# Optimization experiments

Measured on AMD Instinct MI355X. Metric: run time of the kernel, lower is better.

Reference implementation:

```python
import jax, jax.numpy as jnp
import numpy as np

B, T, N, D, H, M = 2, 12, 325, 64, 8, 3
EPS = 1e-6


def _layer_norm(x, g, b):
    mu = jnp.mean(x, axis=-1, keepdims=True)
    var = jnp.mean(jnp.square(x - mu), axis=-1, keepdims=True)
    return (x - mu) * jax.lax.rsqrt(var + EPS) * g + b


def _meta_w(ste, W1, b1, W2, b2):
    # ste: (b,t,n,d) -> per-token weight matrix (b,t,n,d,d)  [Meta_projection]
    h = jax.nn.relu(jnp.einsum('btnd,de->btne', ste, W1) + b1)
    w = jnp.einsum('btnd,df->btnf', h, W2) + b2
    b_, t_, n_, _ = ste.shape
    return w.reshape(b_, t_, n_, D, D)


def _meta_qkv(q, k, v, ste_q, ste_k, ste_v, mW1, mb1, mW2, mb2):
    wq = _meta_w(ste_q, mW1[0], mb1[0], mW2[0], mb2[0])
    wk = _meta_w(ste_k, mW1[1], mb1[1], mW2[1], mb2[1])
    wv = _meta_w(ste_v, mW1[2], mb1[2], mW2[2], mb2[2])
    mg = lambda x, w: jnp.einsum('btnd,btnde->btne', x, w)  # meta_guide
    return mg(q, wq), mg(k, wk), mg(v, wv)


def _split_heads(x):  # (B,L,d) -> (H*B,L,d/H), head-major = tf.concat(tf.split(x,H,-1),0)
    return jnp.concatenate(jnp.split(x, H, axis=-1), axis=0)


def _concat_heads(x):
    return jnp.concatenate(jnp.split(x, H, axis=0), axis=-1)


def _sdpa(q, k, v, tm=None):
    dk = q.shape[-1]
    scores = jnp.einsum('bqd,bkd->bqk', q, k) / jnp.sqrt(jnp.float32(dk))
    if tm is not None:  # spatial mask (n,n) broadcast over batch*heads
        scores = jnp.where(tm[None] > 0, scores, jnp.float32(-1e9))
    att = jax.nn.softmax(scores, axis=-1)
    return jnp.einsum('bqk,bkd->bqd', att, v)


def _temporal_attn(q, k, v, ste_q, ste_k, ste_v, mW1, mb1, mW2, mb2, Wo):
    b, t, n, d = q.shape
    qg, kg, vg = _meta_qkv(q, k, v, ste_q, ste_k, ste_v, mW1, mb1, mW2, mb2)
    rs = lambda x: x.transpose(0, 2, 1, 3).reshape(b * n, t, d)  # temporal_reshape
    out = _sdpa(_split_heads(rs(qg)), _split_heads(rs(kg)), _split_heads(rs(vg)))
    out = _concat_heads(out).reshape(b, n, t, d).transpose(0, 2, 1, 3)
    return jnp.einsum('btnd,de->btne', out, Wo)


def _spatial_attn(q, k, v, tms, ste_q, ste_k, ste_v, mW1, mb1, mW2, mb2, Wo):
    b, t, n, d = q.shape
    # meta weights are identical across the mask loop in the original -> compute once
    qg, kg, vg = _meta_qkv(q, k, v, ste_q, ste_k, ste_v, mW1, mb1, mW2, mb2)
    rs = lambda x: x.reshape(b * t, n, d)  # spatial_reshape
    q_, k_, v_ = _split_heads(rs(qg)), _split_heads(rs(kg)), _split_heads(rs(vg))
    m = tms.shape[0]
    outs = [_concat_heads(_sdpa(q_, k_, v_, tm=tms[i])) for i in range(m)]
    out = jnp.stack(outs).transpose(1, 2, 3, 0).reshape(b, t, n, d * m)
    return jnp.einsum('btnd,de->btne', out, Wo)


def _ffn(x, W1, W2):
    return jax.nn.relu(x @ W1) @ W2


def setup_inputs() -> dict:
    key = jax.random.key(0)
    ks = jax.random.split(key, 16)
    f = lambda i, shape, s=1.0: jax.random.normal(ks[i], shape, dtype=jnp.float32) * s
    return {
        'queries': f(0, (B, T, N, D)),
        'keys': f(1, (B, T, N, D)),
        'values': f(2, (B, T, N, D)),
        'ste_q': f(3, (B, T, N, D)),
        'ste_k': f(4, (B, T, N, D)),
        'ste_v': f(5, (B, T, N, D)),
        'tms': jax.random.randint(ks[6], (M, N, N), 0, 2, dtype=jnp.int32),
        # 4 attention modules (mta1, msa1, mta2, msa2), 3 meta branches each
        'mW1': f(7, (4, 3, D, D), 0.05),
        'mb1': jnp.zeros((4, 3, D), jnp.float32),
        'mW2': f(8, (4, 3, D, D * D), 0.02),
        'mb2': jnp.zeros((4, 3, D * D), jnp.float32),
        'Wo_t': f(9, (2, D, D), 0.05),          # temporal out-proj (no bias)
        'Wo_s': f(10, (2, M * D, D), 0.05),     # spatial out-proj over d*m (no bias)
        'ffn_W1': f(11, (2, D, D // 4), 0.05),
        'ffn_W2': f(12, (2, D // 4, D), 0.05),
        'ln_gamma': jnp.ones((6, D), jnp.float32),
        'ln_beta': jnp.zeros((6, D), jnp.float32),
    }


def reference(queries, keys, values, ste_q, ste_k, ste_v, tms,
              mW1, mb1, mW2, mb2, Wo_t, Wo_s, ffn_W1, ffn_W2, ln_gamma, ln_beta):
    # Encoderlayer with if_ste=True, if_meta=True, training=False (dropout = identity),
    # b_layers=m_layers=t_layers=1.
    tms_f = tms.astype(jnp.float32)
    x = queries
    # --- begin block: temporal attn + LN, spatial attn + LN ---
    out = _temporal_attn(x, keys, values, ste_q, ste_k, ste_v,
                         mW1[0], mb1[0], mW2[0], mb2[0], Wo_t[0])
    x = _layer_norm(x + out, ln_gamma[0], ln_beta[0])
    out = _spatial_attn(x, x, x, tms_f, ste_q, ste_k, ste_v,
                        mW1[1], mb1[1], mW2[1], mb2[1], Wo_s[0])
    x = _layer_norm(x + out, ln_gamma[1], ln_beta[1])
    # --- medium block: temporal + LN, spatial + LN, FFN + LN ---
    out = _temporal_attn(x, x, x, ste_q, ste_k, ste_v,
                         mW1[2], mb1[2], mW2[2], mb2[2], Wo_t[1])
    x = _layer_norm(x + out, ln_gamma[2], ln_beta[2])
    out = _spatial_attn(x, x, x, tms_f, ste_q, ste_k, ste_v,
                        mW1[3], mb1[3], mW2[3], mb2[3], Wo_s[1])
    x = _layer_norm(x + out, ln_gamma[3], ln_beta[3])
    out = _ffn(x, ffn_W1[0], ffn_W2[0])
    x = _layer_norm(x + out, ln_gamma[4], ln_beta[4])
    # --- end block: FFN + LN ---
    out = _ffn(x, ffn_W1[1], ffn_W2[1])
    x = _layer_norm(x + out, ln_gamma[5], ln_beta[5])
    return x
```

## Files before the change

kernel.cpp:

```cpp
#include <hip/hip_runtime.h>
#include <math.h>

#define BB 2
#define TT 12
#define NN 325
#define DD 64
#define HH 8
#define MM 3
#define NT (BB*TT*NN)
#define NT64 (NT*64)
#define EPS 1e-6f
#define KTOT 4160
#define SEGS 8
#define KPS 41
#define NR 328

typedef _Float16 f16x8 __attribute__((ext_vector_type(8)));
typedef _Float16 f16x2 __attribute__((ext_vector_type(2)));
typedef float f32x4 __attribute__((ext_vector_type(4)));
typedef float f32x2 __attribute__((ext_vector_type(2)));

#if __has_builtin(__builtin_amdgcn_exp2f)
#define EXP2F(x) __builtin_amdgcn_exp2f(x)
#else
#define EXP2F(x) exp2f(x)
#endif

__device__ inline float wave_reduce_sum(float v) {
    #pragma unroll
    for (int o = 32; o > 0; o >>= 1) v += __shfl_xor(v, o, 64);
    return v;
}

__global__ __launch_bounds__(256)
void prep_all(const float* __restrict__ mW2, const float* __restrict__ mb2,
              _Float16* __restrict__ Wt,
              const float* __restrict__ mW1, _Float16* __restrict__ W1f,
              const int* __restrict__ tms, unsigned* __restrict__ pmr) {
    const int bx = blockIdx.x;
    const int tid = threadIdx.x;
    if (bx < 780) {
        const int p = bx / 65;
        const int kk0 = (bx % 65) * 64;
        __shared__ float s[64][65];
        #pragma unroll
        for (int pass = 0; pass < 16; ++pass) {
            int idx = pass*256 + tid;
            int kl = idx >> 6, e = idx & 63;
            int kk = kk0 + kl;
            float v = (kk < 4096) ? mW2[(size_t)p*262144 + (size_t)kk*64 + e]
                                  : mb2[(size_t)p*4096 + (size_t)(kk-4096)*64 + e];
            s[kl][e] = v;
        }
        __syncthreads();
        #pragma unroll
        for (int pass = 0; pass < 16; ++pass) {
            int idx = pass*256 + tid;
            int e = idx >> 6, kl = idx & 63;
            Wt[(size_t)p*64*KTOT + (size_t)e*KTOT + kk0 + kl] = (_Float16)s[kl][e];
        }
        return;
    }
    if (bx < 792) {
        const int p = bx - 780;
        #pragma unroll
        for (int i = 0; i < 16; ++i) {
            int idx = i*256 + tid;
            int d = idx >> 6, e = idx & 63;
            W1f[(size_t)p*4096 + e*64 + d] = (_Float16)mW1[(size_t)p*4096 + d*64 + e];
        }
        return;
    }
    int idx = (bx - 792)*256 + tid;
    if (idx >= MM*NN*SEGS) return;
    int seg = idx & 7;
    int nq = (idx >> 3) % NN;
    int i = idx / (SEGS*NN);
    int ks = seg*KPS;
    int ke = (ks + KPS < NN) ? ks + KPS : NN;
    const int* row = tms + ((size_t)i*NN + nq)*NN;
    unsigned w0 = 0, w1 = 0;
    for (int k = ks; k < ke; ++k) {
        int b = k - ks;
        unsigned bit = (row[k] > 0) ? 1u : 0u;
        if (b < 32) w0 |= bit << b; else w1 |= bit << (b - 32);
    }
    pmr[(size_t)idx*2]     = w0;
    pmr[(size_t)idx*2 + 1] = w1;
}

template<int MODE>
__global__ __launch_bounds__(256, 2)
void meta_gemm_t(const float* __restrict__ x0, const float* __restrict__ x1,
                 const float* __restrict__ x2,
                 const float* __restrict__ s0, const float* __restrict__ s1,
                 const float* __restrict__ s2,
                 const _Float16* __restrict__ W1f, const float* __restrict__ b1m,
                 const _Float16* __restrict__ Wtm,
                 void* __restrict__ o0, void* __restrict__ o1, void* __restrict__ o2) {
    const int br = blockIdx.y;
    const int t0 = blockIdx.x * 64;
    const float* xg = (br==0) ? x0 : (br==1) ? x1 : x2;
    const float* sg = (br==0) ? s0 : (br==1) ? s1 : s2;
    const _Float16* W1b = W1f + (size_t)br*4096;
    const float* b1g = b1m + (size_t)br*64;
    const _Float16* W = Wtm + (size_t)br*64*KTOT;
    void* outp = (br==0) ? o0 : (br==1) ? o1 : o2;

    __shared__ _Float16 sx[64*64];
    __shared__ _Float16 ss[64*64];
    __shared__ _Float16 shT[64*68];
    __shared__ _Float16 bB[2][1024*8];

    const int tid = threadIdx.x;
    #pragma unroll
    for (int i = 0; i < 2; ++i) {
        int idx = i*256 + tid;
        int row = idx >> 3, u = idx & 7;
        int t = t0 + row;
        int boff = row*128 + ((u*16) ^ ((row & 7) << 4));
        f16x8 xo, so;
        if (t < NT) {
            const float4* xp = (const float4*)(xg + (size_t)t*64 + u*8);
            float4 a = xp[0], b = xp[1];
            f16x8 xv = {(_Float16)a.x,(_Float16)a.y,(_Float16)a.z,(_Float16)a.w,
                        (_Float16)b.x,(_Float16)b.y,(_Float16)b.z,(_Float16)b.w};
            const float4* sp = (const float4*)(sg + (size_t)t*64 + u*8);
            float4 c = sp[0], d = sp[1];
            f16x8 sv = {(_Float16)c.x,(_Float16)c.y,(_Float16)c.z,(_Float16)c.w,
                        (_Float16)d.x,(_Float16)d.y,(_Float16)d.z,(_Float16)d.w};
            xo = xv; so = sv;
        } else {
            f16x8 z = {(_Float16)0.f,(_Float16)0.f,(_Float16)0.f,(_Float16)0.f,
                       (_Float16)0.f,(_Float16)0.f,(_Float16)0.f,(_Float16)0.f};
            xo = z; so = z;
        }
        *(f16x8*)((char*)sx + boff) = xo;
        *(f16x8*)((char*)ss + boff) = so;
    }
    __syncthreads();

    const int wid = tid >> 6, lane = tid & 63;
    const int col = lane & 15, g = lane >> 4;
    const int wm = wid & 1, wn = wid >> 1;
    const int trow0 = wm*32 + col;
    const int trow1 = trow0 + 16;
    const int rb0 = trow0*128, rb1 = trow1*128;
    const int sz = (trow0 & 7) << 4;

    {
        const int hrow = wid*16 + col;
        const int hrb = hrow*128;
        const int hsz = (hrow & 7) << 4;
        f32x4 ha[4] = {{0,0,0,0},{0,0,0,0},{0,0,0,0},{0,0,0,0}};
        #pragma unroll
        for (int ph = 0; ph < 2; ++ph) {
            int dd = ph*32 + g*8;
            f16x8 sv = *(f16x8*)((char*)ss + hrb + ((dd*2) ^ hsz));
            #pragma unroll
            for (int ni = 0; ni < 4; ++ni) {
                f16x8 bw = *(const f16x8*)(W1b + (size_t)(ni*16+col)*64 + dd);
                ha[ni] = __builtin_amdgcn_mfma_f32_16x16x32_f16(sv, bw, ha[ni], 0, 0, 0);
            }
        }
        #pragma unroll
        for (int ni = 0; ni < 4; ++ni) {
            float bv = b1g[ni*16+col];
            #pragma unroll
            for (int r = 0; r < 4; ++r)
                shT[(wid*16 + g*4 + r)*68 + ni*16 + col] = (_Float16)fmaxf(ha[ni][r] + bv, 0.f);
        }
    }

    f16x8 xv00 = *(f16x8*)((char*)sx + rb0 + (((g*8)*2) ^ sz));
    f16x8 xv01 = *(f16x8*)((char*)sx + rb0 + (((32 + g*8)*2) ^ sz));
    f16x8 xv10 = *(f16x8*)((char*)sx + rb1 + (((g*8)*2) ^ sz));
    f16x8 xv11 = *(f16x8*)((char*)sx + rb1 + (((32 + g*8)*2) ^ sz));

    auto STAGE2 = [&](int bi, int st2) {
        const _Float16* base = W + (size_t)st2*128;
        #pragma unroll
        for (int j = 0; j < 4; ++j) {
            int p = j*256 + tid;
            int t = p >> 9;
            int rest = p & 511;
            int e = rest >> 3, wu = rest & 7;
            const _Float16* src = base + (size_t)t*64 + (size_t)e*KTOT + ((wu ^ (e & 7)) << 3);
            __builtin_amdgcn_global_load_lds(
                (const __attribute__((address_space(1))) void*)src,
                (__attribute__((address_space(3))) void*)&bB[bi][p*8],
                16, 0, 0);
        }
    };
    auto STAGE1 = [&](int bi, int st) {
        const _Float16* base = W + (size_t)st*64;
        #pragma unroll
        for (int j = 0; j < 2; ++j) {
            int p = j*256 + tid;
            int e = p >> 3, wu = p & 7;
            const _Float16* src = base + (size_t)e*KTOT + ((wu ^ (e & 7)) << 3);
            __builtin_amdgcn_global_load_lds(
                (const __attribute__((address_space(1))) void*)src,
                (__attribute__((address_space(3))) void*)&bB[bi][p*8],
                16, 0, 0);
        }
    };

    STAGE2(0, 0);
    STAGE2(1, 1);
    asm volatile("s_waitcnt lgkmcnt(0)" ::: "memory");
    __builtin_amdgcn_sched_barrier(0);

    f32x4 A[2][2] = {{{0,0,0,0},{0,0,0,0}},{{0,0,0,0},{0,0,0,0}}};
    f16x8 hv0 = {}, hv1 = {};

    const int e0 = wn*32 + col;
    const int e1 = e0 + 16;
    const int u00 = e0*8 + (g ^ (e0 & 7));
    const int u01 = e0*8 + ((4 + g) ^ (e0 & 7));
    const int u10 = e1*8 + (g ^ (e1 & 7));
    const int u11 = e1*8 + ((4 + g) ^ (e1 & 7));

    auto COMPUTE = [&](const _Float16* Bb, int ci) {
        #pragma unroll
        for (int t = 0; t < 2; ++t) {
            _Float16 hc0 = hv0[ci*2 + t];
            _Float16 hc1 = hv1[ci*2 + t];
            const _Float16* Bs = Bb + t*512*8;
            f16x8 b00 = *(const f16x8*)((const char*)Bs + u00*16);
            f16x8 b01 = *(const f16x8*)((const char*)Bs + u01*16);
            f16x8 b10 = *(const f16x8*)((const char*)Bs + u10*16);
            f16x8 b11 = *(const f16x8*)((const char*)Bs + u11*16);
            f16x8 p00 = xv00 * hc0;
            f16x8 p10 = xv10 * hc1;
            A[0][0] = __builtin_amdgcn_mfma_f32_16x16x32_f16(p00, b00, A[0][0], 0, 0, 0);
            A[0][1] = __builtin_amdgcn_mfma_f32_16x16x32_f16(p00, b10, A[0][1], 0, 0, 0);
            A[1][0] = __builtin_amdgcn_mfma_f32_16x16x32_f16(p10, b00, A[1][0], 0, 0, 0);
            A[1][1] = __builtin_amdgcn_mfma_f32_16x16x32_f16(p10, b10, A[1][1], 0, 0, 0);
            f16x8 p01 = xv01 * hc0;
            f16x8 p11 = xv11 * hc1;
            A[0][0] = __builtin_amdgcn_mfma_f32_16x16x32_f16(p01, b01, A[0][0], 0, 0, 0);
            A[0][1] = __builtin_amdgcn_mfma_f32_16x16x32_f16(p01, b11, A[0][1], 0, 0, 0);
            A[1][0] = __builtin_amdgcn_mfma_f32_16x16x32_f16(p11, b01, A[1][0], 0, 0, 0);
            A[1][1] = __builtin_amdgcn_mfma_f32_16x16x32_f16(p11, b11, A[1][1], 0, 0, 0);
        }
    };

    for (int q = 0; q < 7; ++q) {
        #pragma unroll
        for (int s = 0; s < 4; ++s) {
            asm volatile("s_waitcnt vmcnt(4)" ::: "memory");
            __builtin_amdgcn_sched_barrier(0);
            __builtin_amdgcn_s_barrier();
            if (s == 0) {
                hv0 = *(f16x8*)&shT[trow0*68 + q*8];
                hv1 = *(f16x8*)&shT[trow1*68 + q*8];
            }
            COMPUTE(bB[s & 1], s);
            __builtin_amdgcn_s_barrier();
            STAGE2(s & 1, 4*q + s + 2);
        }
    }
    asm volatile("s_waitcnt vmcnt(4)" ::: "memory");
    __builtin_amdgcn_sched_barrier(0);
    __builtin_amdgcn_s_barrier();
    hv0 = *(f16x8*)&shT[trow0*68 + 56];
    hv1 = *(f16x8*)&shT[trow1*68 + 56];
    COMPUTE(bB[0], 0);
    __builtin_amdgcn_s_barrier();
    STAGE2(0, 30);

    asm volatile("s_waitcnt vmcnt(4)" ::: "memory");
    __builtin_amdgcn_sched_barrier(0);
    __builtin_amdgcn_s_barrier();
    COMPUTE(bB[1], 1);
    __builtin_amdgcn_s_barrier();
    STAGE2(1, 31);

    asm volatile("s_waitcnt vmcnt(4)" ::: "memory");
    __builtin_amdgcn_sched_barrier(0);
    __builtin_amdgcn_s_barrier();
    COMPUTE(bB[0], 2);
    __builtin_amdgcn_s_barrier();

    asm volatile("s_waitcnt vmcnt(0)" ::: "memory");
    __builtin_amdgcn_sched_barrier(0);
    __builtin_amdgcn_s_barrier();
    COMPUTE(bB[1], 3);
    __builtin_amdgcn_s_barrier();

    STAGE1(0, 64);
    asm volatile("s_waitcnt vmcnt(0)" ::: "memory");
    __builtin_amdgcn_sched_barrier(0);
    __builtin_amdgcn_s_barrier();
    {
        const _Float16* Bs = bB[0];
        f16x8 b00 = *(const f16x8*)((const char*)Bs + u00*16);
        f16x8 b01 = *(const f16x8*)((const char*)Bs + u01*16);
        f16x8 b10 = *(const f16x8*)((const char*)Bs + u10*16);
        f16x8 b11 = *(const f16x8*)((const char*)Bs + u11*16);
        A[0][0] = __builtin_amdgcn_mfma_f32_16x16x32_f16(xv00, b00, A[0][0], 0, 0, 0);
        A[0][1] = __builtin_amdgcn_mfma_f32_16x16x32_f16(xv00, b10, A[0][1], 0, 0, 0);
        A[1][0] = __builtin_amdgcn_mfma_f32_16x16x32_f16(xv10, b00, A[1][0], 0, 0, 0);
        A[1][1] = __builtin_amdgcn_mfma_f32_16x16x32_f16(xv10, b10, A[1][1], 0, 0, 0);
        A[0][0] = __builtin_amdgcn_mfma_f32_16x16x32_f16(xv01, b01, A[0][0], 0, 0, 0);
        A[0][1] = __builtin_amdgcn_mfma_f32_16x16x32_f16(xv01, b11, A[0][1], 0, 0, 0);
        A[1][0] = __builtin_amdgcn_mfma_f32_16x16x32_f16(xv11, b01, A[1][0], 0, 0, 0);
        A[1][1] = __builtin_amdgcn_mfma_f32_16x16x32_f16(xv11, b11, A[1][1], 0, 0, 0);
    }

    if (MODE == 0) {
        float* op = (float*)outp;
        #pragma unroll
        for (int mt = 0; mt < 2; ++mt) {
            #pragma unroll
            for (int nj = 0; nj < 2; ++nj) {
                const int e = e0 + nj*16;
                #pragma unroll
                for (int r = 0; r < 4; ++r) {
                    int t = t0 + wm*32 + mt*16 + g*4 + r;
                    if (t < NT) op[(size_t)t*64 + e] = A[mt][nj][r];
                }
            }
        }
    } else {
        const float KSC = 0.35355339059327373f * 1.4426950408889634f;
        const float scl = (br == 1) ? KSC : 1.f;
        const int bt0 = t0 / NN;
        const int bound = (bt0 + 1)*NN;
        _Float16* op = (_Float16*)outp;
        #pragma unroll
        for (int mt = 0; mt < 2; ++mt) {
            #pragma unroll
            for (int nj = 0; nj < 2; ++nj) {
                const int e = e0 + nj*16;
                const int hh = e >> 3, dd = e & 7;
                #pragma unroll
                for (int r = 0; r < 4; ++r) {
                    int t = t0 + wm*32 + mt*16 + g*4 + r;
                    if (t < NT) {
                        int bt = (t >= bound) ? bt0 + 1 : bt0;
                        int n = t - bt*NN;
                        size_t pidx = ((size_t)(bt*8 + hh)*NR + n)*8 + dd;
                        op[pidx] = (_Float16)(A[mt][nj][r]*scl);
                    }
                }
            }
        }
    }
}

__global__ __launch_bounds__(256)
void temporal_fused(const float* __restrict__ qg, const float* __restrict__ kg,
                    const float* __restrict__ vg, const float* __restrict__ xres,
                    const float* __restrict__ Wo, const float* __restrict__ gamma,
                    const float* __restrict__ beta, float* __restrict__ xout) {
    const int wid = threadIdx.x >> 6, lane = threadIdx.x & 63;
    const int token = blockIdx.x*4 + wid;
    if (token >= NT) return;
    const int n = token % NN;
    const int b = token / (NN*TT);
    const float scale = 0.35355339059327373f;
    const float qv = qg[(size_t)token*64 + lane] * scale;

    float s[TT], v[TT];
    #pragma unroll
    for (int kt = 0; kt < TT; ++kt) {
        size_t base = ((size_t)(b*TT + kt)*NN + n)*64 + lane;
        float kv = kg[base];
        v[kt] = vg[base];
        float d = qv * kv;
        d += __shfl_xor(d, 1, 64);
        d += __shfl_xor(d, 2, 64);
        d += __shfl_xor(d, 4, 64);
        s[kt] = d;
    }
    float m = s[0];
    #pragma unroll
    for (int kt = 1; kt < TT; ++kt) m = fmaxf(m, s[kt]);
    float l = 0.f, O = 0.f;
    #pragma unroll
    for (int kt = 0; kt < TT; ++kt) {
        float p = __expf(s[kt] - m);
        l += p;
        O += p * v[kt];
    }
    O /= l;
    float y = 0.f;
    #pragma unroll
    for (int d = 0; d < 64; ++d) y += __shfl(O, d, 64) * Wo[d*64 + lane];
    float r = xres[(size_t)token*64 + lane] + y;
    float mu = wave_reduce_sum(r) * (1.f/64.f);
    float diff = r - mu;
    float var = wave_reduce_sum(diff*diff) * (1.f/64.f);
    xout[(size_t)token*64 + lane] = diff * rsqrtf(var + EPS) * gamma[lane] + beta[lane];
}

__global__ __launch_bounds__(256)
void spatial_attn13(const _Float16* __restrict__ Qh, const _Float16* __restrict__ Kh,
                    const _Float16* __restrict__ Vh, const unsigned* __restrict__ pmr,
                    _Float16* __restrict__ outs) {
    const int bh = blockIdx.x;
    const int bt = bh >> 3, h = bh & 7;
    const int q0 = blockIdx.y * 32;
    __shared__ _Float16 KV[NR*16];
    const int tid = threadIdx.x;
    const _Float16* Kb = Kh + (size_t)bh*NR*8;
    const _Float16* Vb = Vh + (size_t)bh*NR*8;

    for (int u = tid; u < NR; u += 256) {
        *(f16x8*)&KV[u*16]     = *(const f16x8*)&Kb[u*8];
        *(f16x8*)&KV[u*16 + 8] = *(const f16x8*)&Vb[u*8];
    }
    __syncthreads();

    const int wid = tid >> 6, lane = tid & 63;
    const int qu = lane >> 3, seg = lane & 7;
    const int nq = q0 + wid*8 + qu;
    const bool act = nq < NN;
    const int qm = act ? nq : NN-1;

    f16x8 qv = *(const f16x8*)(Qh + ((size_t)bh*NR + qm)*8);
    const f16x2* qh2 = (const f16x2*)&qv;
    const int ks = seg*KPS;

    const size_t mbase = ((size_t)qm*SEGS + seg)*2;
    const size_t mstep = (size_t)NN*SEGS*2;
    unsigned w00 = pmr[mbase],           w01 = pmr[mbase+1];
    unsigned w10 = pmr[mstep+mbase],     w11 = pmr[mstep+mbase+1];
    unsigned w20 = pmr[2*mstep+mbase],   w21 = pmr[2*mstep+mbase+1];

    float l0 = 0.f, l1 = 0.f, l2 = 0.f;
    f32x2 O0[4] = {{0,0},{0,0},{0,0},{0,0}};
    f32x2 O1[4] = {{0,0},{0,0},{0,0},{0,0}};
    f32x2 O2[4] = {{0,0},{0,0},{0,0},{0,0}};

    f16x8 kc = *(const f16x8*)&KV[ks*16];
    f16x8 vc = *(const f16x8*)&KV[ks*16 + 8];

    auto step = [&](int j, unsigned b0, unsigned b1, unsigned b2) {
        f16x8 kn = kc, vn = vc;
        if (j + 1 < KPS) {
            kn = *(const f16x8*)&KV[(ks + j + 1)*16];
            vn = *(const f16x8*)&KV[(ks + j + 1)*16 + 8];
        }
        const f16x2* k2 = (const f16x2*)&kc;
        float d = __builtin_amdgcn_fdot2(qh2[0], k2[0], -32.f, false);
        d = __builtin_amdgcn_fdot2(qh2[1], k2[1], d, false);
        d = __builtin_amdgcn_fdot2(qh2[2], k2[2], d, false);
        d = __builtin_amdgcn_fdot2(qh2[3], k2[3], d, false);
        float E = EXP2F(d);
        float E0 = b0 ? E : 0.f;
        float E1 = b1 ? E : 0.f;
        float E2 = b2 ? E : 0.f;
        l0 += E0; l1 += E1; l2 += E2;
        f32x2 e0 = {E0, E0}, e1 = {E1, E1}, e2 = {E2, E2};
        #pragma unroll
        for (int jj = 0; jj < 4; ++jj) {
            f32x2 vp = {(float)vc[2*jj], (float)vc[2*jj+1]};
            O0[jj] += e0 * vp;
            O1[jj] += e1 * vp;
            O2[jj] += e2 * vp;
        }
        kc = kn; vc = vn;
    };
    #pragma unroll
    for (int j = 0; j < 32; ++j)
        step(j, (w00 >> j) & 1u, (w10 >> j) & 1u, (w20 >> j) & 1u);
    #pragma unroll
    for (int j = 32; j < KPS; ++j)
        step(j, (w01 >> (j-32)) & 1u, (w11 >> (j-32)) & 1u, (w21 >> (j-32)) & 1u);

    #pragma unroll
    for (int off = 1; off <= 4; off <<= 1) {
        l0 += __shfl_xor(l0, off, 64);
        l1 += __shfl_xor(l1, off, 64);
        l2 += __shfl_xor(l2, off, 64);
        #pragma unroll
        for (int j = 0; j < 4; ++j) {
            #pragma unroll
            for (int c = 0; c < 2; ++c) {
                O0[j][c] += __shfl_xor(O0[j][c], off, 64);
                O1[j][c] += __shfl_xor(O1[j][c], off, 64);
                O2[j][c] += __shfl_xor(O2[j][c], off, 64);
            }
        }
    }

    if (act && seg == 0) {
        float i0 = 1.f/l0, i1 = 1.f/l1, i2 = 1.f/l2;
        _Float16* op = outs + (size_t)(bt*NN + nq)*192 + h*8;
        f16x8 o0, o1, o2;
        #pragma unroll
        for (int j = 0; j < 4; ++j) {
            o0[2*j] = (_Float16)(O0[j][0]*i0); o0[2*j+1] = (_Float16)(O0[j][1]*i0);
            o1[2*j] = (_Float16)(O1[j][0]*i1); o1[2*j+1] = (_Float16)(O1[j][1]*i1);
            o2[2*j] = (_Float16)(O2[j][0]*i2); o2[2*j+1] = (_Float16)(O2[j][1]*i2);
        }
        *(f16x8*)(op)       = o0;
        *(f16x8*)(op + 64)  = o1;
        *(f16x8*)(op + 128) = o2;
    }
}

__global__ __launch_bounds__(256)
void proj_res_ln_s_kernel(const _Float16* __restrict__ a, const float* __restrict__ xres,
                          const float* __restrict__ Wo, const float* __restrict__ gamma,
                          const float* __restrict__ beta, float* __restrict__ xout) {
    const int wid = threadIdx.x >> 6, lane = threadIdx.x & 63;
    const int token = blockIdx.x*4 + wid;
    if (token >= NT) return;
    const _Float16* ap = a + (size_t)token*192;
    const float a0 = (float)ap[lane];
    const float a1 = (float)ap[64 + lane];
    const float a2 = (float)ap[128 + lane];
    float y = 0.f;
    #pragma unroll
    for (int d = 0; d < 64; ++d) {
        y += __shfl(a0, d, 64) * Wo[(d*3+0)*64 + lane];
        y += __shfl(a1, d, 64) * Wo[(d*3+1)*64 + lane];
        y += __shfl(a2, d, 64) * Wo[(d*3+2)*64 + lane];
    }
    float r = xres[(size_t)token*64 + lane] + y;
    float mu = wave_reduce_sum(r) * (1.f/64.f);
    float diff = r - mu;
    float var = wave_reduce_sum(diff*diff) * (1.f/64.f);
    xout[(size_t)token*64 + lane] = diff * rsqrtf(var + EPS) * gamma[lane] + beta[lane];
}

__global__ __launch_bounds__(256)
void tail_fused(const _Float16* __restrict__ a, const float* __restrict__ xres,
                const float* __restrict__ Wo,
                const float* __restrict__ W1a, const float* __restrict__ W2a,
                const float* __restrict__ W1b, const float* __restrict__ W2b,
                const float* __restrict__ ln_g, const float* __restrict__ ln_b,
                float* __restrict__ out) {
    const int wid = threadIdx.x >> 6, lane = threadIdx.x & 63;
    const int token = blockIdx.x*4 + wid;
    if (token >= NT) return;
    const int c = lane & 15;

    const _Float16* ap = a + (size_t)token*192;
    const float a0 = (float)ap[lane];
    const float a1 = (float)ap[64 + lane];
    const float a2 = (float)ap[128 + lane];
    float y = 0.f;
    #pragma unroll
    for (int d = 0; d < 64; ++d) {
        y += __shfl(a0, d, 64) * Wo[(d*3+0)*64 + lane];
        y += __shfl(a1, d, 64) * Wo[(d*3+1)*64 + lane];
        y += __shfl(a2, d, 64) * Wo[(d*3+2)*64 + lane];
    }
    float r = xres[(size_t)token*64 + lane] + y;
    float mu = wave_reduce_sum(r) * (1.f/64.f);
    float diff = r - mu;
    float var = wave_reduce_sum(diff*diff) * (1.f/64.f);
    float x1 = diff * rsqrtf(var + EPS) * ln_g[lane] + ln_b[lane];

    float hs = 0.f;
    #pragma unroll
    for (int d = 0; d < 64; ++d) hs += __shfl(x1, d, 64) * W1a[d*16 + c];
    float hr = fmaxf(hs, 0.f);
    float y2 = 0.f;
    #pragma unroll
    for (int cc = 0; cc < 16; ++cc) y2 += __shfl(hr, cc, 64) * W2a[cc*64 + lane];
    r = x1 + y2;
    mu = wave_reduce_sum(r) * (1.f/64.f);
    diff = r - mu;
    var = wave_reduce_sum(diff*diff) * (1.f/64.f);
    float x2 = diff * rsqrtf(var + EPS) * ln_g[64 + lane] + ln_b[64 + lane];

    hs = 0.f;
    #pragma unroll
    for (int d = 0; d < 64; ++d) hs += __shfl(x2, d, 64) * W1b[d*16 + c];
    hr = fmaxf(hs, 0.f);
    y2 = 0.f;
    #pragma unroll
    for (int cc = 0; cc < 16; ++cc) y2 += __shfl(hr, cc, 64) * W2b[cc*64 + lane];
    r = x2 + y2;
    mu = wave_reduce_sum(r) * (1.f/64.f);
    diff = r - mu;
    var = wave_reduce_sum(diff*diff) * (1.f/64.f);
    out[(size_t)token*64 + lane] = diff * rsqrtf(var + EPS) * ln_g[128 + lane] + ln_b[128 + lane];
}

extern "C" void kernel_launch(void* const* d_in, const int* in_sizes, int n_in,
                              void* d_out, int out_size, void* d_ws, size_t ws_size,
                              hipStream_t stream) {
    const float* queries = (const float*)d_in[0];
    const float* keys    = (const float*)d_in[1];
    const float* values  = (const float*)d_in[2];
    const float* ste_q   = (const float*)d_in[3];
    const float* ste_k   = (const float*)d_in[4];
    const float* ste_v   = (const float*)d_in[5];
    const int*   tms     = (const int*)d_in[6];
    const float* mW1     = (const float*)d_in[7];
    const float* mb1     = (const float*)d_in[8];
    const float* mW2     = (const float*)d_in[9];
    const float* mb2     = (const float*)d_in[10];
    const float* Wo_t    = (const float*)d_in[11];
    const float* Wo_s    = (const float*)d_in[12];
    const float* ffn_W1  = (const float*)d_in[13];
    const float* ffn_W2  = (const float*)d_in[14];
    const float* ln_g    = (const float*)d_in[15];
    const float* ln_b    = (const float*)d_in[16];

    char* p = (char*)d_ws;
    auto carve = [&](size_t bytes) { char* r = p; p += (bytes + 255) & ~(size_t)255; return r; };
    float* xbuf = (float*)carve((size_t)NT64*4);
    float* qg   = (float*)carve((size_t)NT64*4);
    float* kg   = (float*)carve((size_t)NT64*4);
    float* vg   = (float*)carve((size_t)NT64*4);
    _Float16* as_ = (_Float16*)carve((size_t)NT*192*2);
    _Float16* Wt  = (_Float16*)carve((size_t)12*64*KTOT*2);
    _Float16* W1f = (_Float16*)carve((size_t)12*4096*2);
    unsigned* pmr = (unsigned*)carve((size_t)MM*NN*SEGS*2*4);
    _Float16* Qh  = (_Float16*)carve((size_t)BB*TT*HH*NR*8*2);
    _Float16* Kh  = (_Float16*)carve((size_t)BB*TT*HH*NR*8*2);
    _Float16* Vh  = (_Float16*)carve((size_t)BB*TT*HH*NR*8*2);

    const dim3 blk(256);
    const dim3 g_tok(NT/4);
    const dim3 g_sa(BB*TT*HH, 11);
    const dim3 g_gemm((NT + 63)/64, 3);

    prep_all<<<dim3(823), blk, 0, stream>>>(mW2, mb2, Wt, mW1, W1f, tms, pmr);

    meta_gemm_t<0><<<g_gemm, blk, 0, stream>>>(
        queries, keys, values, ste_q, ste_k, ste_v,
        W1f, mb1, Wt, (void*)qg, (void*)kg, (void*)vg);
    temporal_fused<<<g_tok, blk, 0, stream>>>(
        qg, kg, vg, queries, Wo_t, ln_g, ln_b, xbuf);

    meta_gemm_t<1><<<g_gemm, blk, 0, stream>>>(
        xbuf, xbuf, xbuf, ste_q, ste_k, ste_v,
        W1f + (size_t)3*4096, mb1 + (size_t)3*64, Wt + (size_t)3*64*KTOT,
        (void*)Qh, (void*)Kh, (void*)Vh);
    spatial_attn13<<<g_sa, blk, 0, stream>>>(Qh, Kh, Vh, pmr, as_);
    proj_res_ln_s_kernel<<<g_tok, blk, 0, stream>>>(
        as_, xbuf, Wo_s, ln_g + 64, ln_b + 64, xbuf);

    meta_gemm_t<0><<<g_gemm, blk, 0, stream>>>(
        xbuf, xbuf, xbuf, ste_q, ste_k, ste_v,
        W1f + (size_t)6*4096, mb1 + (size_t)6*64, Wt + (size_t)6*64*KTOT,
        (void*)qg, (void*)kg, (void*)vg);
    temporal_fused<<<g_tok, blk, 0, stream>>>(
        qg, kg, vg, xbuf, Wo_t + (size_t)64*64, ln_g + 128, ln_b + 128, xbuf);

    meta_gemm_t<1><<<g_gemm, blk, 0, stream>>>(
        xbuf, xbuf, xbuf, ste_q, ste_k, ste_v,
        W1f + (size_t)9*4096, mb1 + (size_t)9*64, Wt + (size_t)9*64*KTOT,
        (void*)Qh, (void*)Kh, (void*)Vh);
    spatial_attn13<<<g_sa, blk, 0, stream>>>(Qh, Kh, Vh, pmr, as_);
    tail_fused<<<g_tok, blk, 0, stream>>>(
        as_, xbuf, Wo_s + (size_t)192*64,
        ffn_W1, ffn_W2, ffn_W1 + (size_t)64*16, ffn_W2 + (size_t)16*64,
        ln_g + 192, ln_b + 192, (float*)d_out);
}
```

Measured before the change: 243.8 us.

## Use triple-buffered LDS staging to drop one barrier per K-step

The meta-weight GEMM's LDS staging buffer grows from two to three slots. The next stage is now issued right after the barrier and before compute, so each step needs one barrier instead of two. The main loop is restructured into 12-step unrolled chunks so the slot index (mod 3) stays a compile-time constant, and the final single-stage tile gets its own slot so it can be prefetched earlier. This costs about 16KB more shared memory per block, which may lower occupancy.

```diff
diff --git a/kernel.cpp b/kernel.cpp
--- a/kernel.cpp
+++ b/kernel.cpp
@@ -110,7 +110,7 @@
     __shared__ _Float16 sx[64*64];
     __shared__ _Float16 ss[64*64];
     __shared__ _Float16 shT[64*68];
-    __shared__ _Float16 bB[2][1024*8];
+    __shared__ _Float16 bB[3][1024*8];
 
     const int tid = threadIdx.x;
     #pragma unroll
@@ -177,7 +177,7 @@
     f16x8 xv10 = *(f16x8*)((char*)sx + rb1 + (((g*8)*2) ^ sz));
     f16x8 xv11 = *(f16x8*)((char*)sx + rb1 + (((32 + g*8)*2) ^ sz));
 
-    auto STAGE2 = [&](int bi, int st2) {
+    auto STAGE2 = [&](int slot, int st2) {
         const _Float16* base = W + (size_t)st2*128;
         #pragma unroll
         for (int j = 0; j < 4; ++j) {
@@ -188,11 +188,11 @@
             const _Float16* src = base + (size_t)t*64 + (size_t)e*KTOT + ((wu ^ (e & 7)) << 3);
             __builtin_amdgcn_global_load_lds(
                 (const __attribute__((address_space(1))) void*)src,
-                (__attribute__((address_space(3))) void*)&bB[bi][p*8],
+                (__attribute__((address_space(3))) void*)&bB[slot][p*8],
                 16, 0, 0);
         }
     };
-    auto STAGE1 = [&](int bi, int st) {
+    auto STAGE1 = [&](int slot, int st) {
         const _Float16* base = W + (size_t)st*64;
         #pragma unroll
         for (int j = 0; j < 2; ++j) {
@@ -201,7 +201,7 @@
             const _Float16* src = base + (size_t)e*KTOT + ((wu ^ (e & 7)) << 3);
             __builtin_amdgcn_global_load_lds(
                 (const __attribute__((address_space(1))) void*)src,
-                (__attribute__((address_space(3))) void*)&bB[bi][p*8],
+                (__attribute__((address_space(3))) void*)&bB[slot][p*8],
                 16, 0, 0);
         }
     };
@@ -246,55 +246,48 @@
         }
     };
 
-    for (int q = 0; q < 7; ++q) {
-        #pragma unroll
-        for (int s = 0; s < 4; ++s) {
+    for (int q = 0; q < 2; ++q) {
+        const int hb0 = trow0*68 + q*24;
+        const int hb1 = trow1*68 + q*24;
+        #pragma unroll
+        for (int s = 0; s < 12; ++s) {
             asm volatile("s_waitcnt vmcnt(4)" ::: "memory");
             __builtin_amdgcn_sched_barrier(0);
             __builtin_amdgcn_s_barrier();
-            if (s == 0) {
-                hv0 = *(f16x8*)&shT[trow0*68 + q*8];
-                hv1 = *(f16x8*)&shT[trow1*68 + q*8];
+            if ((s & 3) == 0) {
+                hv0 = *(f16x8*)&shT[hb0 + s*2];
+                hv1 = *(f16x8*)&shT[hb1 + s*2];
             }
-            COMPUTE(bB[s & 1], s);
-            __builtin_amdgcn_s_barrier();
-            STAGE2(s & 1, 4*q + s + 2);
-        }
+            STAGE2((s + 2) % 3, 12*q + s + 2);
+            COMPUTE(bB[s % 3], s & 3);
+        }
+    }
+    #pragma unroll
+    for (int s = 24; s < 30; ++s) {
+        asm volatile("s_waitcnt vmcnt(4)" ::: "memory");
+        __builtin_amdgcn_sched_barrier(0);
+        __builtin_amdgcn_s_barrier();
+        if ((s & 3) == 0) {
+            hv0 = *(f16x8*)&shT[trow0*68 + s*2];
+            hv1 = *(f16x8*)&shT[trow1*68 + s*2];
+        }
+        STAGE2((s + 2) % 3, s + 2);
+        COMPUTE(bB[s % 3], s & 3);
     }
     asm volatile("s_waitcnt vmcnt(4)" ::: "memory");
     __builtin_amdgcn_sched_barrier(0);
     __builtin_amdgcn_s_barrier();
-    hv0 = *(f16x8*)&shT[trow0*68 + 56];
-    hv1 = *(f16x8*)&shT[trow1*68 + 56];
-    COMPUTE(bB[0], 0);
-    __builtin_amdgcn_s_barrier();
-    STAGE2(0, 30);
-
-    asm volatile("s_waitcnt vmcnt(4)" ::: "memory");
-    __builtin_amdgcn_sched_barrier(0);
-    __builtin_amdgcn_s_barrier();
-    COMPUTE(bB[1], 1);
-    __builtin_amdgcn_s_barrier();
-    STAGE2(1, 31);
-
-    asm volatile("s_waitcnt vmcnt(4)" ::: "memory");
-    __builtin_amdgcn_sched_barrier(0);
-    __builtin_amdgcn_s_barrier();
+    STAGE1(2, 64);
     COMPUTE(bB[0], 2);
-    __builtin_amdgcn_s_barrier();
-
-    asm volatile("s_waitcnt vmcnt(0)" ::: "memory");
+    asm volatile("s_waitcnt vmcnt(2)" ::: "memory");
     __builtin_amdgcn_sched_barrier(0);
     __builtin_amdgcn_s_barrier();
     COMPUTE(bB[1], 3);
-    __builtin_amdgcn_s_barrier();
-
-    STAGE1(0, 64);
     asm volatile("s_waitcnt vmcnt(0)" ::: "memory");
     __builtin_amdgcn_sched_barrier(0);
     __builtin_amdgcn_s_barrier();
     {
-        const _Float16* Bs = bB[0];
+        const _Float16* Bs = bB[2];
         f16x8 b00 = *(const f16x8*)((const char*)Bs + u00*16);
         f16x8 b01 = *(const f16x8*)((const char*)Bs + u01*16);
         f16x8 b10 = *(const f16x8*)((const char*)Bs + u10*16);
```

Result: slower. 252.0 us (+3.4%).
